# Optimization experiments

Hardware: AMD Instinct MI355X
Metric: run time of the kernel (lower is better)

The kernel has to match this reference:

```python
import jax, jax.numpy as jnp
import numpy as np

N_WIRES = 8  # d_k = embed_dim // num_heads
# Fixed realization of tq.RandomLayer(n_ops=8): 6 param rotations + 2 CNOTs
RANDOM_OPS = [("rx", 0), ("ry", 3), ("rz", 5), ("cnot", (1, 2)),
              ("rx", 6), ("ry", 7), ("cnot", (4, 0)), ("rz", 2)]


def _apply_rot(state, kind, theta, wire, n):
    # state: (N,) + (2,)*n complex; theta: scalar or (N,)
    a = jnp.moveaxis(state, 1 + wire, -1)
    if jnp.ndim(theta) == 1:
        theta = theta.reshape((-1,) + (1,) * (n - 1))
    half = theta * 0.5
    a0, a1 = a[..., 0], a[..., 1]
    if kind == "rx":
        c, s = jnp.cos(half), jnp.sin(half)
        n0 = c * a0 - 1j * s * a1
        n1 = -1j * s * a0 + c * a1
    elif kind == "ry":
        c, s = jnp.cos(half), jnp.sin(half)
        n0 = c * a0 - s * a1
        n1 = s * a0 + c * a1
    else:  # rz
        n0 = jnp.exp(-1j * half) * a0
        n1 = jnp.exp(1j * half) * a1
    a = jnp.stack([n0, n1], axis=-1)
    return jnp.moveaxis(a, -1, 1 + wire)


def _apply_cnot(state, ctrl, tgt, n):
    a = jnp.moveaxis(state, (1 + ctrl, 1 + tgt), (-2, -1))  # (..., 2c, 2t)
    a = jnp.stack([a[..., 0, :], a[..., 1, ::-1]], axis=-2)
    return jnp.moveaxis(a, (-2, -1), (1 + ctrl, 1 + tgt))


def run_circuit(flat, q_params):
    # flat: (N, n_wires) float angles -> (N, n_wires) PauliZ expectations
    n = N_WIRES
    N = flat.shape[0]
    state = jnp.zeros((N, 2 ** n), dtype=jnp.complex64).at[:, 0].set(1.0)
    state = state.reshape((N,) + (2,) * n)
    # RX encoder: angle flat[:, i] on wire i
    for i in range(n):
        state = _apply_rot(state, "rx", flat[:, i], i, n)
    # random layer (fixed realization)
    p = 0
    for kind, w in RANDOM_OPS:
        if kind == "cnot":
            state = _apply_cnot(state, w[0], w[1], n)
        else:
            state = _apply_rot(state, kind, q_params[p], w, n)
            p += 1
    # MeasureAll(PauliZ): <Z_i> = P(bit_i=0) - P(bit_i=1)
    probs = jnp.abs(state) ** 2  # (N, 2,...,2)
    exps = []
    for i in range(n):
        axes = tuple(ax for ax in range(1, n + 1) if ax != 1 + i)
        marg = probs.sum(axis=axes)  # (N, 2)
        exps.append(marg[:, 0] - marg[:, 1])
    return jnp.stack(exps, axis=-1)  # (N, n)


def setup_inputs() -> dict:
    key = jax.random.key(0)
    k1, k2, k3, k4 = jax.random.split(key, 4)
    B, S, E = 8, 1024, 64
    return {
        "x": jax.random.normal(k1, (B, S, E), dtype=jnp.float32),
        "W_combine": jax.random.normal(k2, (E, E), dtype=jnp.float32) * (1.0 / np.sqrt(E)),
        "b_combine": jax.random.normal(k3, (E,), dtype=jnp.float32) * 0.02,
        "q_params": jax.random.normal(k4, (6,), dtype=jnp.float32),
    }


def reference(x, W_combine, b_combine, q_params):
    B, S, E = x.shape
    H = E // N_WIRES  # num_heads
    d_k = N_WIRES
    # Heads share the same qlayer params, so batch all heads through one pass;
    # per-head slicing + restacking in the original is order-equivalent.
    flat = x.reshape(B * S * H, d_k)
    q_out = run_circuit(flat, q_params)  # (B*S*H, d_k)
    out = q_out.reshape(B, S, E)
    return out @ W_combine.T + b_combine
```

## Files before the change

kernel.cpp:

```cpp
#include <hip/hip_runtime.h>


#define BLOCK 256
#define WAVES 4
#define ROWS_PER_WAVE 4
#define ROWS_PER_BLOCK (WAVES * ROWS_PER_WAVE)

__global__ __launch_bounds__(BLOCK) void qattn_kernel(
    const float* __restrict__ x,
    const float* __restrict__ W,
    const float* __restrict__ bvec,
    const float* __restrict__ qp,
    float* __restrict__ out,
    int nrows)
{
    __shared__ float qbuf[WAVES][64];

    const int lane = threadIdx.x & 63;
    const int wv   = threadIdx.x >> 6;

    float4 wreg[16];
    const float4* W4 = reinterpret_cast<const float4*>(W + lane * 64);
    #pragma unroll
    for (int kk = 0; kk < 16; ++kk) wreg[kk] = W4[kk];

    const float bias = bvec[lane];
    const float p0 = qp[0], p1 = qp[1], p3 = qp[3], p4 = qp[4];
    const float cp1 = __cosf(p1);
    const float cp4 = __cosf(p4);

    const int i    = lane & 7;
    const int base = lane & ~7;
    const float add = (i == 0) ? p0 : (i == 6) ? p3 : 0.0f;

    const int row0 = (blockIdx.x * WAVES + wv) * ROWS_PER_WAVE;

    #pragma unroll
    for (int r = 0; r < ROWS_PER_WAVE; ++r) {
        const int row = row0 + r;
        if (row >= nrows) break;

        const float xv  = x[row * 64 + lane];
        const float xo4 = __shfl(xv, base + 4, 64);
        const float xo1 = __shfl(xv, base + 1, 64);
        float fac = 1.0f;
        if      (i == 0) fac = __cosf(xo4);
        else if (i == 2) fac = __cosf(xo1);
        else if (i == 3) fac = cp1;
        else if (i == 7) fac = cp4;
        const float q = fac * __cosf(xv + add);

        qbuf[wv][lane] = q;

        float acc = bias;
        const float4* q4 = reinterpret_cast<const float4*>(qbuf[wv]);
        #pragma unroll
        for (int kk = 0; kk < 16; ++kk) {
            const float4 qq = q4[kk];
            acc = fmaf(qq.x, wreg[kk].x, acc);
            acc = fmaf(qq.y, wreg[kk].y, acc);
            acc = fmaf(qq.z, wreg[kk].z, acc);
            acc = fmaf(qq.w, wreg[kk].w, acc);
        }
        out[row * 64 + lane] = acc;
    }
}

extern "C" void kernel_launch(void* const* d_in, const int* in_sizes, int n_in,
                              void* d_out, int out_size, void* d_ws, size_t ws_size,
                              hipStream_t stream) {
    const float* x  = (const float*)d_in[0];
    const float* W  = (const float*)d_in[1];
    const float* b  = (const float*)d_in[2];
    const float* qp = (const float*)d_in[3];
    float* out = (float*)d_out;

    const int nrows  = in_sizes[0] / 64;
    const int blocks = (nrows + ROWS_PER_BLOCK - 1) / ROWS_PER_BLOCK;

    qattn_kernel<<<blocks, BLOCK, 0, stream>>>(x, W, b, qp, out, nrows);
}
```

Measured before the change: 12.66 us.

## Load four rows per wave as float4 and batch the matvec across rows

Each lane now loads one float4 covering four consecutive elements, so a wave reads all four of its rows in a single vectorized load. The cosine-product features are computed with one xor shuffle that relies on the 8-wire pattern lining up with float4 boundaries. The 64x64 matvec then reuses each register-held W chunk across four row accumulators, which cuts the per-row loop overhead and raises instruction-level parallelism. In exchange the per-row bounds check is dropped, so it assumes nrows is a multiple of four.

```diff
diff --git a/kernel.cpp b/kernel.cpp
--- a/kernel.cpp
+++ b/kernel.cpp
@@ -14,7 +14,7 @@
     float* __restrict__ out,
     int nrows)
 {
-    __shared__ float qbuf[WAVES][64];
+    __shared__ float qbuf[WAVES][ROWS_PER_WAVE * 64];
 
     const int lane = threadIdx.x & 63;
     const int wv   = threadIdx.x >> 6;
@@ -29,41 +29,46 @@
     const float cp1 = __cosf(p1);
     const float cp4 = __cosf(p4);
 
-    const int i    = lane & 7;
-    const int base = lane & ~7;
-    const float add = (i == 0) ? p0 : (i == 6) ? p3 : 0.0f;
+    const int   parity = lane & 1;
+    const float add0 = parity ? 0.0f : p0;
+    const float add2 = parity ? p3 : 0.0f;
+    const float wfac = parity ? cp4 : cp1;
 
     const int row0 = (blockIdx.x * WAVES + wv) * ROWS_PER_WAVE;
+    if (row0 >= nrows) return;
+
+    const float4 v = reinterpret_cast<const float4*>(x + row0 * 64)[lane];
+
+    const float c0 = __cosf(v.x + add0);
+    const float c1 = __cosf(v.y);
+    const float c2 = __cosf(v.z + add2);
+    const float c3 = __cosf(v.w);
+    const float other = __shfl_xor(c0, 1, 64);
+
+    float4 q;
+    q.x = parity ? c0 : other * c0;
+    q.y = c1;
+    q.z = parity ? c2 : c1 * c2;
+    q.w = wfac * c3;
+
+    reinterpret_cast<float4*>(qbuf[wv])[lane] = q;
+
+    float acc[ROWS_PER_WAVE] = {bias, bias, bias, bias};
+    #pragma unroll
+    for (int kk = 0; kk < 16; ++kk) {
+        #pragma unroll
+        for (int r = 0; r < ROWS_PER_WAVE; ++r) {
+            const float4 qq = reinterpret_cast<const float4*>(qbuf[wv] + r * 64)[kk];
+            acc[r] = fmaf(qq.x, wreg[kk].x, acc[r]);
+            acc[r] = fmaf(qq.y, wreg[kk].y, acc[r]);
+            acc[r] = fmaf(qq.z, wreg[kk].z, acc[r]);
+            acc[r] = fmaf(qq.w, wreg[kk].w, acc[r]);
+        }
+    }
 
     #pragma unroll
-    for (int r = 0; r < ROWS_PER_WAVE; ++r) {
-        const int row = row0 + r;
-        if (row >= nrows) break;
-
-        const float xv  = x[row * 64 + lane];
-        const float xo4 = __shfl(xv, base + 4, 64);
-        const float xo1 = __shfl(xv, base + 1, 64);
-        float fac = 1.0f;
-        if      (i == 0) fac = __cosf(xo4);
-        else if (i == 2) fac = __cosf(xo1);
-        else if (i == 3) fac = cp1;
-        else if (i == 7) fac = cp4;
-        const float q = fac * __cosf(xv + add);
-
-        qbuf[wv][lane] = q;
-
-        float acc = bias;
-        const float4* q4 = reinterpret_cast<const float4*>(qbuf[wv]);
-        #pragma unroll
-        for (int kk = 0; kk < 16; ++kk) {
-            const float4 qq = q4[kk];
-            acc = fmaf(qq.x, wreg[kk].x, acc);
-            acc = fmaf(qq.y, wreg[kk].y, acc);
-            acc = fmaf(qq.z, wreg[kk].z, acc);
-            acc = fmaf(qq.w, wreg[kk].w, acc);
-        }
-        out[row * 64 + lane] = acc;
-    }
+    for (int r = 0; r < ROWS_PER_WAVE; ++r)
+        out[(row0 + r) * 64 + lane] = acc[r];
 }
 
 extern "C" void kernel_launch(void* const* d_in, const int* in_sizes, int n_in,
```

Result: slower. 16.05 us (+26.7%).

## Split wave into half-waves processing two rows each with 2x2 register tiling

Applied to the files above, without the earlier changes.

Each wave now handles its four rows as two passes of two rows at once, one row per half-wave. Each lane holds two W rows and computes a 2x2 tile of outputs, so every LDS read of q is reused across two output columns. All x loads are issued up front, before the W loads, and the cos of the neighbour wire is shared through shuffles instead of being recomputed. The trade-off is more registers (two W rows per lane), mitigated by a launch_bounds hint. It also drops the per-row nrows bounds check, which assumes nrows is a multiple of four.

```diff
diff --git a/kernel.cpp b/kernel.cpp
--- a/kernel.cpp
+++ b/kernel.cpp
@@ -6,7 +6,7 @@
 #define ROWS_PER_WAVE 4
 #define ROWS_PER_BLOCK (WAVES * ROWS_PER_WAVE)
 
-__global__ __launch_bounds__(BLOCK) void qattn_kernel(
+__global__ __launch_bounds__(BLOCK, 2) void qattn_kernel(
     const float* __restrict__ x,
     const float* __restrict__ W,
     const float* __restrict__ bvec,
@@ -14,56 +14,87 @@
     float* __restrict__ out,
     int nrows)
 {
-    __shared__ float qbuf[WAVES][64];
+    __shared__ float qbuf[WAVES][2][2][64];
 
     const int lane = threadIdx.x & 63;
     const int wv   = threadIdx.x >> 6;
+    const int half = lane >> 5;
+    const int l5   = lane & 31;
 
-    float4 wreg[16];
-    const float4* W4 = reinterpret_cast<const float4*>(W + lane * 64);
+    const int row0 = (blockIdx.x * WAVES + wv) * ROWS_PER_WAVE;
+    if (row0 >= nrows) return;
+
+    const int rA = row0 + half;
+    const int rB = row0 + 2 + half;
+
+    const float xa0 = x[rA * 64 + l5];
+    const float xb0 = x[rA * 64 + l5 + 32];
+    const float xa1 = x[rB * 64 + l5];
+    const float xb1 = x[rB * 64 + l5 + 32];
+
+    float4 wregA[16], wregB[16];
+    const float4* WA = reinterpret_cast<const float4*>(W + l5 * 64);
+    const float4* WB = reinterpret_cast<const float4*>(W + (l5 + 32) * 64);
     #pragma unroll
-    for (int kk = 0; kk < 16; ++kk) wreg[kk] = W4[kk];
+    for (int kk = 0; kk < 16; ++kk) { wregA[kk] = WA[kk]; wregB[kk] = WB[kk]; }
 
-    const float bias = bvec[lane];
+    const float biasA = bvec[l5];
+    const float biasB = bvec[l5 + 32];
     const float p0 = qp[0], p1 = qp[1], p3 = qp[3], p4 = qp[4];
     const float cp1 = __cosf(p1);
     const float cp4 = __cosf(p4);
 
-    const int i    = lane & 7;
-    const int base = lane & ~7;
-    const float add = (i == 0) ? p0 : (i == 6) ? p3 : 0.0f;
+    const int   i    = l5 & 7;
+    const float add  = (i == 0) ? p0 : (i == 6) ? p3 : 0.0f;
+    const float cfac = (i == 3) ? cp1 : (i == 7) ? cp4 : 1.0f;
+    const int   src4 = (lane & 56) | 4;
+    const int   src1 = (lane & 56) | 1;
 
-    const int row0 = (blockIdx.x * WAVES + wv) * ROWS_PER_WAVE;
+    const float ca0 = __cosf(xa0 + add), cb0 = __cosf(xb0 + add);
+    const float s4a0 = __shfl(ca0, src4, 64), s4b0 = __shfl(cb0, src4, 64);
+    const float s1a0 = __shfl(ca0, src1, 64), s1b0 = __shfl(cb0, src1, 64);
+    const float fa0 = (i == 0) ? s4a0 : (i == 2) ? s1a0 : cfac;
+    const float fb0 = (i == 0) ? s4b0 : (i == 2) ? s1b0 : cfac;
+    qbuf[wv][0][half][l5]      = fa0 * ca0;
+    qbuf[wv][0][half][l5 + 32] = fb0 * cb0;
 
+    const float ca1 = __cosf(xa1 + add), cb1 = __cosf(xb1 + add);
+    const float s4a1 = __shfl(ca1, src4, 64), s4b1 = __shfl(cb1, src4, 64);
+    const float s1a1 = __shfl(ca1, src1, 64), s1b1 = __shfl(cb1, src1, 64);
+    const float fa1 = (i == 0) ? s4a1 : (i == 2) ? s1a1 : cfac;
+    const float fb1 = (i == 0) ? s4b1 : (i == 2) ? s1b1 : cfac;
+    qbuf[wv][1][half][l5]      = fa1 * ca1;
+    qbuf[wv][1][half][l5 + 32] = fb1 * cb1;
+
+    float accA0 = biasA, accB0 = biasB, accA1 = biasA, accB1 = biasB;
+    const float4* q0 = reinterpret_cast<const float4*>(qbuf[wv][0][half]);
+    const float4* q1 = reinterpret_cast<const float4*>(qbuf[wv][1][half]);
     #pragma unroll
-    for (int r = 0; r < ROWS_PER_WAVE; ++r) {
-        const int row = row0 + r;
-        if (row >= nrows) break;
+    for (int kk = 0; kk < 16; ++kk) {
+        const float4 a = q0[kk];
+        const float4 b = q1[kk];
+        accA0 = fmaf(a.x, wregA[kk].x, accA0);
+        accA0 = fmaf(a.y, wregA[kk].y, accA0);
+        accA0 = fmaf(a.z, wregA[kk].z, accA0);
+        accA0 = fmaf(a.w, wregA[kk].w, accA0);
+        accB0 = fmaf(a.x, wregB[kk].x, accB0);
+        accB0 = fmaf(a.y, wregB[kk].y, accB0);
+        accB0 = fmaf(a.z, wregB[kk].z, accB0);
+        accB0 = fmaf(a.w, wregB[kk].w, accB0);
+        accA1 = fmaf(b.x, wregA[kk].x, accA1);
+        accA1 = fmaf(b.y, wregA[kk].y, accA1);
+        accA1 = fmaf(b.z, wregA[kk].z, accA1);
+        accA1 = fmaf(b.w, wregA[kk].w, accA1);
+        accB1 = fmaf(b.x, wregB[kk].x, accB1);
+        accB1 = fmaf(b.y, wregB[kk].y, accB1);
+        accB1 = fmaf(b.z, wregB[kk].z, accB1);
+        accB1 = fmaf(b.w, wregB[kk].w, accB1);
+    }
 
-        const float xv  = x[row * 64 + lane];
-        const float xo4 = __shfl(xv, base + 4, 64);
-        const float xo1 = __shfl(xv, base + 1, 64);
-        float fac = 1.0f;
-        if      (i == 0) fac = __cosf(xo4);
-        else if (i == 2) fac = __cosf(xo1);
-        else if (i == 3) fac = cp1;
-        else if (i == 7) fac = cp4;
-        const float q = fac * __cosf(xv + add);
-
-        qbuf[wv][lane] = q;
-
-        float acc = bias;
-        const float4* q4 = reinterpret_cast<const float4*>(qbuf[wv]);
-        #pragma unroll
-        for (int kk = 0; kk < 16; ++kk) {
-            const float4 qq = q4[kk];
-            acc = fmaf(qq.x, wreg[kk].x, acc);
-            acc = fmaf(qq.y, wreg[kk].y, acc);
-            acc = fmaf(qq.z, wreg[kk].z, acc);
-            acc = fmaf(qq.w, wreg[kk].w, acc);
-        }
-        out[row * 64 + lane] = acc;
-    }
+    out[rA * 64 + l5]      = accA0;
+    out[rA * 64 + l5 + 32] = accB0;
+    out[rB * 64 + l5]      = accA1;
+    out[rB * 64 + l5 + 32] = accB1;
 }
 
 extern "C" void kernel_launch(void* const* d_in, const int* in_sizes, int n_in,
```

Measured after the change: 13.70 us. 1.08x slower.
